# Kernel tuning notes

Measured on AMD Instinct MI355X. Metric: run time of the kernel, lower is better.

## Reference

```python
import jax, jax.numpy as jnp
import numpy as np

B, T, I, H = 32768, 18, 2, 64  # batch, seq_len (forced by fc2 in_features=18), input_dim, hidden_dim


def setup_inputs() -> dict:
    key = jax.random.key(0)
    ks = jax.random.split(key, 13)
    s = 1.0 / np.sqrt(H)  # torch default GRU/Linear init scale
    return {
        "x": jax.random.normal(ks[0], (B, T, I), jnp.float32),
        "w_ih_f": jax.random.uniform(ks[1], (3 * H, I), jnp.float32, -s, s),
        "w_hh_f": jax.random.uniform(ks[2], (3 * H, H), jnp.float32, -s, s),
        "b_ih_f": jax.random.uniform(ks[3], (3 * H,), jnp.float32, -s, s),
        "b_hh_f": jax.random.uniform(ks[4], (3 * H,), jnp.float32, -s, s),
        "w_ih_b": jax.random.uniform(ks[5], (3 * H, I), jnp.float32, -s, s),
        "w_hh_b": jax.random.uniform(ks[6], (3 * H, H), jnp.float32, -s, s),
        "b_ih_b": jax.random.uniform(ks[7], (3 * H,), jnp.float32, -s, s),
        "b_hh_b": jax.random.uniform(ks[8], (3 * H,), jnp.float32, -s, s),
        "fc1_w": jax.random.uniform(ks[9], (24, 2 * H), jnp.float32, -s, s),
        "fc1_b": jax.random.uniform(ks[10], (24,), jnp.float32, -s, s),
        "fc2_w": jax.random.uniform(ks[11], (2, T), jnp.float32, -s, s),
        "fc2_b": jax.random.uniform(ks[12], (2,), jnp.float32, -s, s),
    }


def _gru_scan(x_proj, w_hh, b_hh):
    """x_proj: (T, B, 3H) precomputed input projections. Returns (T, B, H)."""
    h0 = jnp.zeros((x_proj.shape[1], w_hh.shape[1]), x_proj.dtype)

    def step(h, xp):
        gh = h @ w_hh.T + b_hh
        i_r, i_z, i_n = jnp.split(xp, 3, axis=-1)
        h_r, h_z, h_n = jnp.split(gh, 3, axis=-1)
        r = jax.nn.sigmoid(i_r + h_r)
        z = jax.nn.sigmoid(i_z + h_z)
        n = jnp.tanh(i_n + r * h_n)
        h_new = (1 - z) * n + z * h
        return h_new, h_new

    _, hs = jax.lax.scan(step, h0, x_proj)
    return hs


def reference(x, w_ih_f, w_hh_f, b_ih_f, b_hh_f,
              w_ih_b, w_hh_b, b_ih_b, b_hh_b,
              fc1_w, fc1_b, fc2_w, fc2_b):
    # precompute input-gate projections for both directions: (T, B, 3H)
    xp_f = jnp.einsum('bti,gi->tbg', x, w_ih_f) + b_ih_f
    xp_b = jnp.einsum('bti,gi->tbg', x[:, ::-1], w_ih_b) + b_ih_b
    hf = _gru_scan(xp_f, w_hh_f, b_hh_f)           # (T, B, H)
    hb = _gru_scan(xp_b, w_hh_b, b_hh_b)[::-1]     # (T, B, H), re-aligned to forward time
    out = jnp.concatenate([hf, hb], axis=-1).transpose(1, 0, 2)  # (B, T, 2H)
    out = out @ fc1_w.T + fc1_b                    # (B, T, 24)
    out = out.reshape(out.shape[0], 24, -1)        # (B, 24, T) raw row-major reshape, as in torch
    out = out @ fc2_w.T + fc2_b                    # (B, 24, 2)
    return out
```

## Files before the change

kernel.cpp:

```cpp
#include <hip/hip_runtime.h>

#define TT 18

typedef __attribute__((ext_vector_type(8))) short short8;
typedef __attribute__((ext_vector_type(4))) float float4_t;
typedef __attribute__((ext_vector_type(2))) unsigned int uint2_t;

static __device__ __forceinline__ float frcp(float x){ return __builtin_amdgcn_rcpf(x); }
static __device__ __forceinline__ float sigm(float x){ return frcp(1.f + __expf(-x)); }
static __device__ __forceinline__ float tanh_fast(float x){ return fmaf(2.f, frcp(1.f + __expf(-2.f*x)), -1.f); }
static __device__ __forceinline__ unsigned rne_bits(float f){
    unsigned u = __float_as_uint(f);
    return u + 0x7fffu + ((u >> 16) & 1u);
}
static __device__ __forceinline__ void bsplit(float f, unsigned &hi, unsigned &lo){
    unsigned rb = rne_bits(f);
    hi = rb >> 16;
    float fh = __uint_as_float(rb & 0xffff0000u);
    lo = rne_bits(f - fh) >> 16;
}
static __device__ __forceinline__ unsigned pack_hi16(unsigned hi_src, unsigned lo_src){
#if defined(__has_builtin)
#if __has_builtin(__builtin_amdgcn_perm)
    return __builtin_amdgcn_perm(hi_src, lo_src, 0x07060302u);
#else
    return (lo_src >> 16) | (hi_src & 0xffff0000u);
#endif
#else
    return (lo_src >> 16) | (hi_src & 0xffff0000u);
#endif
}

union U8 { short8 s; unsigned u[4]; };

__global__ __launch_bounds__(256) void head_precompute(
    const float* __restrict__ fc1_w, const float* __restrict__ fc1_b,
    const float* __restrict__ fc2_w, const float* __restrict__ fc2_b,
    unsigned short* __restrict__ Bhi, unsigned short* __restrict__ Blo,
    float* __restrict__ Cvec)
{
    int idx = blockIdx.x * 256 + threadIdx.x;
    if (idx < 24 * 2 * 18 * 128) {
        int jg = idx & 127;
        int t  = (idx >> 7) % 18;
        int k  = (idx / 2304) & 1;
        int r  = idx / 4608;
        float acc = 0.f;
        for (int c = 0; c < 24; ++c) {
            int s = t * 24 + c - r * 18;
            if (s >= 0 && s < 18) acc += fc2_w[k * 18 + s] * fc1_w[c * 128 + jg];
        }
        unsigned hi, lo;
        bsplit(acc, hi, lo);
        Bhi[idx] = (unsigned short)hi;
        Blo[idx] = (unsigned short)lo;
    }
    if (idx < 48) {
        int k = idx & 1, r = idx >> 1;
        float acc = fc2_b[k];
        for (int s = 0; s < 18; ++s)
            acc += fc2_w[k * 18 + s] * fc1_b[(r * 18 + s) % 24];
        Cvec[idx] = acc;
    }
}

struct SMv {
    alignas(16) unsigned short hb[2][2][1024];
    uint2_t x2[16][18];
    float out_acc[16][49];
};

__global__ __launch_bounds__(256, 4) void gru_mfma(
    const float* __restrict__ x,
    const float* __restrict__ w_ih_f, const float* __restrict__ w_hh_f,
    const float* __restrict__ b_ih_f, const float* __restrict__ b_hh_f,
    const float* __restrict__ w_ih_b, const float* __restrict__ w_hh_b,
    const float* __restrict__ b_ih_b, const float* __restrict__ b_hh_b,
    const unsigned short* __restrict__ Bhi, const unsigned short* __restrict__ Blo,
    const float* __restrict__ Cvec, float* __restrict__ out)
{
    __shared__ SMv sm;
    const int tid  = threadIdx.x;
    const int lane = tid & 63;
    const int jq   = tid >> 6;
    const int col  = lane & 15;
    const int quad = lane >> 4;
    const int bi   = blockIdx.x;
    const int dir  = bi >> 11;
    const int bb   = (bi & 2047) * 16;
    const bool q0  = (quad == 0);

    const float* __restrict__ wih = dir ? w_ih_b : w_ih_f;
    const float* __restrict__ whh = dir ? w_hh_b : w_hh_f;
    const float* __restrict__ bih = dir ? b_ih_b : b_ih_f;
    const float* __restrict__ bhh = dir ? b_hh_b : b_hh_f;

    #pragma unroll
    for (int p = tid; p < 288; p += 256) {
        int b = p / 18, t = p % 18;
        const float* xp = x + (size_t)(bb + b) * 36 + t * 2;
        unsigned h0, l0, h1, l1;
        bsplit(xp[0], h0, l0);
        bsplit(xp[1], h1, l1);
        uint2_t s2; s2[0] = h0 | (l0 << 16); s2[1] = h1 | (l1 << 16);
        sm.x2[b][t] = s2;
    }
    {
        unsigned* z = (unsigned*)&sm.hb[1][0][0];
        #pragma unroll
        for (int o = 0; o < 4; ++o) z[tid + o * 256] = 0u;
    }
    for (int o = tid; o < 16 * 49; o += 256) ((float*)sm.out_acc)[o] = 0.f;

    short8 wf[3][2];
    #pragma unroll
    for (int ty = 0; ty < 3; ++ty) {
        int g = ty * 64 + jq * 16 + col;
        #pragma unroll
        for (int c = 0; c < 2; ++c) {
            const float* p = whh + g * 64 + c * 32 + quad * 8;
            float4_t f0 = *(const float4_t*)p;
            float4_t f1 = *(const float4_t*)(p + 4);
            short8 s;
            #pragma unroll
            for (int e = 0; e < 8; ++e) {
                float f = (e < 4) ? f0[e] : f1[e - 4];
                s[e] = (short)(rne_bits(f) >> 16);
            }
            wf[ty][c] = s;
        }
    }

    short8 c2[4];
    {
        #pragma unroll
        for (int ty = 0; ty < 2; ++ty) {
            int g = ty * 64 + jq * 16 + col;
            unsigned w0h, w0l, w1h, w1l, bh, bl;
            bsplit(wih[2 * g],     w0h, w0l);
            bsplit(wih[2 * g + 1], w1h, w1l);
            bsplit(bih[g] + bhh[g], bh, bl);
            U8 f;
            f.u[0] = q0 ? (w0h | (w0h << 16)) : 0u;
            f.u[1] = q0 ? (w0l | (w1h << 16)) : 0u;
            f.u[2] = q0 ? (w1h | (w1l << 16)) : 0u;
            f.u[3] = q0 ? (bh  | (bl  << 16)) : 0u;
            c2[ty] = f.s;
        }
        int g = 128 + jq * 16 + col;
        unsigned w0h, w0l, w1h, w1l, bxh, bxl, bhh_h, bhh_l;
        bsplit(wih[2 * g],     w0h, w0l);
        bsplit(wih[2 * g + 1], w1h, w1l);
        bsplit(bih[g], bxh, bxl);
        bsplit(bhh[g], bhh_h, bhh_l);
        U8 fn;
        fn.u[0] = 0u; fn.u[1] = 0u; fn.u[2] = 0u;
        fn.u[3] = q0 ? (bhh_h | (bhh_l << 16)) : 0u;
        c2[2] = fn.s;
        U8 fx;
        fx.u[0] = q0 ? (w0h | (w0h << 16)) : 0u;
        fx.u[1] = q0 ? (w0l | (w1h << 16)) : 0u;
        fx.u[2] = q0 ? (w1h | (w1l << 16)) : 0u;
        fx.u[3] = q0 ? (bxh | (bxl << 16)) : 0u;
        c2[3] = fx.s;
    }

    float hprev[4] = {0.f, 0.f, 0.f, 0.f};

    __syncthreads();

    auto step = [&](int t, int pr, int pw) {
        const bool myhead = (t > 0) && (((t - 1) & 3) == jq);

        int ta_h = 0, base_h = 0;
        size_t boff = 0;
        short8 hA0, hA1, lA0, lA1, hfl0, hfl1;
        if (myhead) {
            int s  = t - 1;
            ta_h   = dir ? (TT - 1 - s) : s;
            base_h = 4 * (ta_h / 3) + ta_h % 3;
            int i  = col & 3;
            int rr = base_h + (i >> 1);
            int kk = i & 1;
            boff = (size_t)((rr * 2 + kk) * TT + ta_h) * 128 + dir * 64 + quad * 8;
            hA0 = *(const short8*)(Bhi + boff);
            hA1 = *(const short8*)(Bhi + boff + 32);
            hfl0 = *(const short8*)&sm.hb[pr][1][(0 * 4 + quad) * 128 + col * 8];
            hfl1 = *(const short8*)&sm.hb[pr][1][(1 * 4 + quad) * 128 + col * 8];
        }

        short8 hfh[2];
        #pragma unroll
        for (int c = 0; c < 2; ++c)
            hfh[c] = *(const short8*)&sm.hb[pr][0][(c * 4 + quad) * 128 + col * 8];

        const int tx = dir ? (TT - 1 - t) : t;
        short8 b2f;
        {
            uint2_t xs = sm.x2[col][tx];
            U8 B;
            B.u[0] = q0 ? xs[0] : 0u;
            B.u[1] = q0 ? ((xs[0] & 0xffffu) | (xs[1] << 16)) : 0u;
            B.u[2] = q0 ? ((xs[1] >> 16) | (xs[1] << 16)) : 0u;
            B.u[3] = q0 ? 0x3F803F80u : 0u;
            b2f = B.s;
        }

        float4_t aR  = (float4_t){0.f,0.f,0.f,0.f};
        float4_t aZ  = (float4_t){0.f,0.f,0.f,0.f};
        float4_t aNH = (float4_t){0.f,0.f,0.f,0.f};
        float4_t aNX = (float4_t){0.f,0.f,0.f,0.f};
        #pragma unroll
        for (int c = 0; c < 2; ++c) {
            aR  = __builtin_amdgcn_mfma_f32_16x16x32_bf16(wf[0][c], hfh[c], aR,  0, 0, 0);
            aZ  = __builtin_amdgcn_mfma_f32_16x16x32_bf16(wf[1][c], hfh[c], aZ,  0, 0, 0);
            aNH = __builtin_amdgcn_mfma_f32_16x16x32_bf16(wf[2][c], hfh[c], aNH, 0, 0, 0);
        }
        aR  = __builtin_amdgcn_mfma_f32_16x16x32_bf16(c2[0], b2f, aR,  0, 0, 0);
        aZ  = __builtin_amdgcn_mfma_f32_16x16x32_bf16(c2[1], b2f, aZ,  0, 0, 0);
        aNH = __builtin_amdgcn_mfma_f32_16x16x32_bf16(c2[2], b2f, aNH, 0, 0, 0);
        aNX = __builtin_amdgcn_mfma_f32_16x16x32_bf16(c2[3], b2f, aNX, 0, 0, 0);

        unsigned rh[4], rl[4];
        #pragma unroll
        for (int reg = 0; reg < 4; ++reg) {
            float r = sigm(aR[reg]);
            float z = sigm(aZ[reg]);
            float n = tanh_fast(fmaf(r, aNH[reg], aNX[reg]));
            float hnew = fmaf(z, hprev[reg] - n, n);
            hprev[reg] = hnew;
            unsigned rb = rne_bits(hnew);
            rh[reg] = rb;
            float fh = __uint_as_float(rb & 0xffff0000u);
            rl[reg] = rne_bits(hnew - fh);
        }
        int woff = (jq * 2 + (quad >> 1)) * 128 + col * 8 + (quad & 1) * 4;
        uint2_t dh, dl;
        dh[0] = pack_hi16(rh[1], rh[0]);
        dh[1] = pack_hi16(rh[3], rh[2]);
        dl[0] = pack_hi16(rl[1], rl[0]);
        dl[1] = pack_hi16(rl[3], rl[2]);
        *(uint2_t*)&sm.hb[pw][0][woff] = dh;
        *(uint2_t*)&sm.hb[pw][1][woff] = dl;

        if (myhead) {
            lA0 = *(const short8*)(Blo + boff);
            lA1 = *(const short8*)(Blo + boff + 32);
            float4_t acch = (float4_t){0.f,0.f,0.f,0.f};
            acch = __builtin_amdgcn_mfma_f32_16x16x32_bf16(hA0, hfh[0], acch, 0, 0, 0);
            acch = __builtin_amdgcn_mfma_f32_16x16x32_bf16(hA1, hfh[1], acch, 0, 0, 0);
            acch = __builtin_amdgcn_mfma_f32_16x16x32_bf16(hA0, hfl0,   acch, 0, 0, 0);
            acch = __builtin_amdgcn_mfma_f32_16x16x32_bf16(hA1, hfl1,   acch, 0, 0, 0);
            acch = __builtin_amdgcn_mfma_f32_16x16x32_bf16(lA0, hfh[0], acch, 0, 0, 0);
            acch = __builtin_amdgcn_mfma_f32_16x16x32_bf16(lA1, hfh[1], acch, 0, 0, 0);
            if (q0) {
                #pragma unroll
                for (int reg = 0; reg < 4; ++reg) {
                    int r2 = base_h + (reg >> 1);
                    sm.out_acc[col][r2 * 2 + (reg & 1)] += acch[reg];
                }
            }
        }
        __syncthreads();
    };

    #pragma unroll 1
    for (int tt = 0; tt < 9; ++tt) {
        step(2 * tt,     1, 0);
        step(2 * tt + 1, 0, 1);
    }

    if (jq == ((TT - 1) & 3)) {
        int s  = TT - 1;
        int ta = dir ? 0 : s;
        int base_h = 4 * (ta / 3) + ta % 3;
        int i  = col & 3;
        int rr = base_h + (i >> 1);
        int kk = i & 1;
        size_t boff = (size_t)((rr * 2 + kk) * TT + ta) * 128 + dir * 64 + quad * 8;
        short8 hA0 = *(const short8*)(Bhi + boff);
        short8 hA1 = *(const short8*)(Bhi + boff + 32);
        short8 lA0 = *(const short8*)(Blo + boff);
        short8 lA1 = *(const short8*)(Blo + boff + 32);
        short8 hfh0 = *(const short8*)&sm.hb[1][0][(0 * 4 + quad) * 128 + col * 8];
        short8 hfh1 = *(const short8*)&sm.hb[1][0][(1 * 4 + quad) * 128 + col * 8];
        short8 hfl0 = *(const short8*)&sm.hb[1][1][(0 * 4 + quad) * 128 + col * 8];
        short8 hfl1 = *(const short8*)&sm.hb[1][1][(1 * 4 + quad) * 128 + col * 8];
        float4_t acch = (float4_t){0.f,0.f,0.f,0.f};
        acch = __builtin_amdgcn_mfma_f32_16x16x32_bf16(hA0, hfh0, acch, 0, 0, 0);
        acch = __builtin_amdgcn_mfma_f32_16x16x32_bf16(hA1, hfh1, acch, 0, 0, 0);
        acch = __builtin_amdgcn_mfma_f32_16x16x32_bf16(hA0, hfl0, acch, 0, 0, 0);
        acch = __builtin_amdgcn_mfma_f32_16x16x32_bf16(hA1, hfl1, acch, 0, 0, 0);
        acch = __builtin_amdgcn_mfma_f32_16x16x32_bf16(lA0, hfh0, acch, 0, 0, 0);
        acch = __builtin_amdgcn_mfma_f32_16x16x32_bf16(lA1, hfh1, acch, 0, 0, 0);
        if (q0) {
            #pragma unroll
            for (int reg = 0; reg < 4; ++reg) {
                int r2 = base_h + (reg >> 1);
                sm.out_acc[col][r2 * 2 + (reg & 1)] += acch[reg];
            }
        }
    }
    __syncthreads();

    #pragma unroll
    for (int rep = 0; rep < 3; ++rep) {
        int o = rep * 256 + tid;
        int b = o / 48, c = o % 48;
        atomicAdd(&out[(size_t)bb * 48 + o], sm.out_acc[b][c] + 0.5f * Cvec[c]);
    }
}

extern "C" void kernel_launch(void* const* d_in, const int* in_sizes, int n_in,
                              void* d_out, int out_size, void* d_ws, size_t ws_size,
                              hipStream_t stream) {
    const float* x      = (const float*)d_in[0];
    const float* w_ih_f = (const float*)d_in[1];
    const float* w_hh_f = (const float*)d_in[2];
    const float* b_ih_f = (const float*)d_in[3];
    const float* b_hh_f = (const float*)d_in[4];
    const float* w_ih_b = (const float*)d_in[5];
    const float* w_hh_b = (const float*)d_in[6];
    const float* b_ih_b = (const float*)d_in[7];
    const float* b_hh_b = (const float*)d_in[8];
    const float* fc1_w  = (const float*)d_in[9];
    const float* fc1_b  = (const float*)d_in[10];
    const float* fc2_w  = (const float*)d_in[11];
    const float* fc2_b  = (const float*)d_in[12];
    float* out  = (float*)d_out;

    float*          Cvec = (float*)d_ws;
    unsigned short* Bhi  = (unsigned short*)((char*)d_ws + 256);
    unsigned short* Blo  = Bhi + 110592;

    hipMemsetAsync(d_out, 0, (size_t)out_size * sizeof(float), stream);
    head_precompute<<<432, 256, 0, stream>>>(fc1_w, fc1_b, fc2_w, fc2_b, Bhi, Blo, Cvec);
    gru_mfma<<<4096, 256, 0, stream>>>(x, w_ih_f, w_hh_f, b_ih_f, b_hh_f,
                                       w_ih_b, w_hh_b, b_ih_b, b_hh_b,
                                       Bhi, Blo, Cvec, out);
}
```

Baseline: 194.5 us.

## Prescale gate weights by log2e, stage x/bias fragments in LDS, use exp2

Folds the log2(e) and 2*log2(e) factors into the recurrent, input and bias weights so the gate nonlinearities can call the hardware exp2 directly without an extra multiply. The per-lane constant bias and input-weight fragments and the per-step x operand are moved from registers into shared memory, with one wave building the next step's x fragment ahead of time. This is meant to cut register pressure and per-step VALU packing work. The low half of the h split now skips rounding, and the head-accumulation loads are regrouped into one block. The cost is extra LDS reads every step and slight numerical differences from prescaling weights before the bf16 split.

```diff
diff --git a/kernel.cpp b/kernel.cpp
--- a/kernel.cpp
+++ b/kernel.cpp
@@ -6,9 +6,17 @@
 typedef __attribute__((ext_vector_type(4))) float float4_t;
 typedef __attribute__((ext_vector_type(2))) unsigned int uint2_t;
 
+#if defined(__has_builtin)
+#if __has_builtin(__builtin_amdgcn_exp2f)
+#define FEXP2(x) __builtin_amdgcn_exp2f(x)
+#else
+#define FEXP2(x) exp2f(x)
+#endif
+#else
+#define FEXP2(x) exp2f(x)
+#endif
+
 static __device__ __forceinline__ float frcp(float x){ return __builtin_amdgcn_rcpf(x); }
-static __device__ __forceinline__ float sigm(float x){ return frcp(1.f + __expf(-x)); }
-static __device__ __forceinline__ float tanh_fast(float x){ return fmaf(2.f, frcp(1.f + __expf(-2.f*x)), -1.f); }
 static __device__ __forceinline__ unsigned rne_bits(float f){
     unsigned u = __float_as_uint(f);
     return u + 0x7fffu + ((u >> 16) & 1u);
@@ -32,6 +40,8 @@
 }
 
 union U8 { short8 s; unsigned u[4]; };
+
+#define MFMA16(A,B,C) __builtin_amdgcn_mfma_f32_16x16x32_bf16((A),(B),(C),0,0,0)
 
 __global__ __launch_bounds__(256) void head_precompute(
     const float* __restrict__ fc1_w, const float* __restrict__ fc1_b,
@@ -66,6 +76,9 @@
 
 struct SMv {
     alignas(16) unsigned short hb[2][2][1024];
+    alignas(16) unsigned short b2x[2][64][8];
+    alignas(16) unsigned short c2a[4][4][16][8];
+    alignas(16) unsigned short zero16[8];
     uint2_t x2[16][18];
     float out_acc[16][49];
 };
@@ -95,7 +108,20 @@
     const float* __restrict__ bih = dir ? b_ih_b : b_ih_f;
     const float* __restrict__ bhh = dir ? b_hh_b : b_hh_f;
 
-    #pragma unroll
+    const float L1 = 1.4426950408889634f;
+    const float L2 = 2.8853900817779268f;
+
+    {
+        unsigned* z = (unsigned*)&sm.hb[1][0][0];
+        #pragma unroll
+        for (int o = 0; o < 4; ++o) z[tid + o * 256] = 0u;
+        unsigned* z2 = (unsigned*)&sm.b2x[0][0][0];
+        #pragma unroll
+        for (int o = 0; o < 2; ++o) z2[tid + o * 256] = 0u;
+        if (tid < 4) ((unsigned*)sm.zero16)[tid] = 0u;
+    }
+    for (int o = tid; o < 16 * 49; o += 256) ((float*)sm.out_acc)[o] = 0.f;
+
     for (int p = tid; p < 288; p += 256) {
         int b = p / 18, t = p % 18;
         const float* xp = x + (size_t)(bb + b) * 36 + t * 2;
@@ -105,16 +131,64 @@
         uint2_t s2; s2[0] = h0 | (l0 << 16); s2[1] = h1 | (l1 << 16);
         sm.x2[b][t] = s2;
     }
-    {
-        unsigned* z = (unsigned*)&sm.hb[1][0][0];
-        #pragma unroll
-        for (int o = 0; o < 4; ++o) z[tid + o * 256] = 0u;
-    }
-    for (int o = tid; o < 16 * 49; o += 256) ((float*)sm.out_acc)[o] = 0.f;
+
+    if (tid < 16) {
+        int tx0 = dir ? (TT - 1) : 0;
+        const float* xp = x + (size_t)(bb + tid) * 36 + tx0 * 2;
+        unsigned h0, l0, h1, l1;
+        bsplit(xp[0], h0, l0);
+        bsplit(xp[1], h1, l1);
+        U8 B;
+        B.u[0] = h0 | (l0 << 16);
+        B.u[1] = h0 | (h1 << 16);
+        B.u[2] = l1 | (h1 << 16);
+        B.u[3] = 0x3F803F80u;
+        *(short8*)&sm.b2x[1][tid][0] = B.s;
+    }
+
+    if (q0) {
+        int g0 = jq * 16 + col;
+        #pragma unroll
+        for (int ty = 0; ty < 2; ++ty) {
+            int g = ty * 64 + g0;
+            unsigned w0h, w0l, w1h, w1l, bh, bl;
+            bsplit(L1 * wih[2 * g],     w0h, w0l);
+            bsplit(L1 * wih[2 * g + 1], w1h, w1l);
+            bsplit(L1 * (bih[g] + bhh[g]), bh, bl);
+            U8 f;
+            f.u[0] = w0h | (w0h << 16);
+            f.u[1] = w0l | (w1h << 16);
+            f.u[2] = w1h | (w1l << 16);
+            f.u[3] = bh  | (bl  << 16);
+            *(short8*)&sm.c2a[jq][ty][col][0] = f.s;
+        }
+        {
+            unsigned bh, bl;
+            bsplit(L2 * bhh[128 + g0], bh, bl);
+            U8 f;
+            f.u[0] = 0u; f.u[1] = 0u; f.u[2] = 0u;
+            f.u[3] = bh | (bl << 16);
+            *(short8*)&sm.c2a[jq][2][col][0] = f.s;
+        }
+        {
+            int g = 128 + g0;
+            unsigned w0h, w0l, w1h, w1l, bh, bl;
+            bsplit(L2 * wih[2 * g],     w0h, w0l);
+            bsplit(L2 * wih[2 * g + 1], w1h, w1l);
+            bsplit(L2 * bih[g], bh, bl);
+            U8 f;
+            f.u[0] = w0h | (w0h << 16);
+            f.u[1] = w0l | (w1h << 16);
+            f.u[2] = w1h | (w1l << 16);
+            f.u[3] = bh  | (bl  << 16);
+            *(short8*)&sm.c2a[jq][3][col][0] = f.s;
+        }
+    }
 
     short8 wf[3][2];
     #pragma unroll
     for (int ty = 0; ty < 3; ++ty) {
+        float sc = (ty == 2) ? L2 : L1;
         int g = ty * 64 + jq * 16 + col;
         #pragma unroll
         for (int c = 0; c < 2; ++c) {
@@ -125,114 +199,58 @@
             #pragma unroll
             for (int e = 0; e < 8; ++e) {
                 float f = (e < 4) ? f0[e] : f1[e - 4];
-                s[e] = (short)(rne_bits(f) >> 16);
+                s[e] = (short)(rne_bits(sc * f) >> 16);
             }
             wf[ty][c] = s;
         }
     }
 
-    short8 c2[4];
-    {
-        #pragma unroll
-        for (int ty = 0; ty < 2; ++ty) {
-            int g = ty * 64 + jq * 16 + col;
-            unsigned w0h, w0l, w1h, w1l, bh, bl;
-            bsplit(wih[2 * g],     w0h, w0l);
-            bsplit(wih[2 * g + 1], w1h, w1l);
-            bsplit(bih[g] + bhh[g], bh, bl);
-            U8 f;
-            f.u[0] = q0 ? (w0h | (w0h << 16)) : 0u;
-            f.u[1] = q0 ? (w0l | (w1h << 16)) : 0u;
-            f.u[2] = q0 ? (w1h | (w1l << 16)) : 0u;
-            f.u[3] = q0 ? (bh  | (bl  << 16)) : 0u;
-            c2[ty] = f.s;
-        }
-        int g = 128 + jq * 16 + col;
-        unsigned w0h, w0l, w1h, w1l, bxh, bxl, bhh_h, bhh_l;
-        bsplit(wih[2 * g],     w0h, w0l);
-        bsplit(wih[2 * g + 1], w1h, w1l);
-        bsplit(bih[g], bxh, bxl);
-        bsplit(bhh[g], bhh_h, bhh_l);
-        U8 fn;
-        fn.u[0] = 0u; fn.u[1] = 0u; fn.u[2] = 0u;
-        fn.u[3] = q0 ? (bhh_h | (bhh_l << 16)) : 0u;
-        c2[2] = fn.s;
-        U8 fx;
-        fx.u[0] = q0 ? (w0h | (w0h << 16)) : 0u;
-        fx.u[1] = q0 ? (w0l | (w1h << 16)) : 0u;
-        fx.u[2] = q0 ? (w1h | (w1l << 16)) : 0u;
-        fx.u[3] = q0 ? (bxh | (bxl << 16)) : 0u;
-        c2[3] = fx.s;
-    }
+    const unsigned short* c2p0 = q0 ? &sm.c2a[jq][0][col][0] : sm.zero16;
+    const unsigned short* c2p1 = q0 ? &sm.c2a[jq][1][col][0] : sm.zero16;
+    const unsigned short* c2p2 = q0 ? &sm.c2a[jq][2][col][0] : sm.zero16;
+    const unsigned short* c2p3 = q0 ? &sm.c2a[jq][3][col][0] : sm.zero16;
 
     float hprev[4] = {0.f, 0.f, 0.f, 0.f};
 
     __syncthreads();
 
     auto step = [&](int t, int pr, int pw) {
-        const bool myhead = (t > 0) && (((t - 1) & 3) == jq);
-
-        int ta_h = 0, base_h = 0;
-        size_t boff = 0;
-        short8 hA0, hA1, lA0, lA1, hfl0, hfl1;
-        if (myhead) {
-            int s  = t - 1;
-            ta_h   = dir ? (TT - 1 - s) : s;
-            base_h = 4 * (ta_h / 3) + ta_h % 3;
-            int i  = col & 3;
-            int rr = base_h + (i >> 1);
-            int kk = i & 1;
-            boff = (size_t)((rr * 2 + kk) * TT + ta_h) * 128 + dir * 64 + quad * 8;
-            hA0 = *(const short8*)(Bhi + boff);
-            hA1 = *(const short8*)(Bhi + boff + 32);
-            hfl0 = *(const short8*)&sm.hb[pr][1][(0 * 4 + quad) * 128 + col * 8];
-            hfl1 = *(const short8*)&sm.hb[pr][1][(1 * 4 + quad) * 128 + col * 8];
-        }
-
         short8 hfh[2];
-        #pragma unroll
-        for (int c = 0; c < 2; ++c)
-            hfh[c] = *(const short8*)&sm.hb[pr][0][(c * 4 + quad) * 128 + col * 8];
-
-        const int tx = dir ? (TT - 1 - t) : t;
-        short8 b2f;
-        {
-            uint2_t xs = sm.x2[col][tx];
-            U8 B;
-            B.u[0] = q0 ? xs[0] : 0u;
-            B.u[1] = q0 ? ((xs[0] & 0xffffu) | (xs[1] << 16)) : 0u;
-            B.u[2] = q0 ? ((xs[1] >> 16) | (xs[1] << 16)) : 0u;
-            B.u[3] = q0 ? 0x3F803F80u : 0u;
-            b2f = B.s;
-        }
+        hfh[0] = *(const short8*)&sm.hb[pr][0][quad * 128 + col * 8];
+        hfh[1] = *(const short8*)&sm.hb[pr][0][(4 + quad) * 128 + col * 8];
+        short8 b2f  = *(const short8*)&sm.b2x[pr][lane][0];
+        short8 c2f0 = *(const short8*)c2p0;
+        short8 c2f1 = *(const short8*)c2p1;
+        short8 c2f2 = *(const short8*)c2p2;
+        short8 c2f3 = *(const short8*)c2p3;
 
         float4_t aR  = (float4_t){0.f,0.f,0.f,0.f};
         float4_t aZ  = (float4_t){0.f,0.f,0.f,0.f};
         float4_t aNH = (float4_t){0.f,0.f,0.f,0.f};
         float4_t aNX = (float4_t){0.f,0.f,0.f,0.f};
-        #pragma unroll
-        for (int c = 0; c < 2; ++c) {
-            aR  = __builtin_amdgcn_mfma_f32_16x16x32_bf16(wf[0][c], hfh[c], aR,  0, 0, 0);
-            aZ  = __builtin_amdgcn_mfma_f32_16x16x32_bf16(wf[1][c], hfh[c], aZ,  0, 0, 0);
-            aNH = __builtin_amdgcn_mfma_f32_16x16x32_bf16(wf[2][c], hfh[c], aNH, 0, 0, 0);
-        }
-        aR  = __builtin_amdgcn_mfma_f32_16x16x32_bf16(c2[0], b2f, aR,  0, 0, 0);
-        aZ  = __builtin_amdgcn_mfma_f32_16x16x32_bf16(c2[1], b2f, aZ,  0, 0, 0);
-        aNH = __builtin_amdgcn_mfma_f32_16x16x32_bf16(c2[2], b2f, aNH, 0, 0, 0);
-        aNX = __builtin_amdgcn_mfma_f32_16x16x32_bf16(c2[3], b2f, aNX, 0, 0, 0);
+        aR  = MFMA16(wf[0][0], hfh[0], aR);
+        aR  = MFMA16(wf[0][1], hfh[1], aR);
+        aR  = MFMA16(c2f0,     b2f,    aR);
+        aZ  = MFMA16(wf[1][0], hfh[0], aZ);
+        aZ  = MFMA16(wf[1][1], hfh[1], aZ);
+        aZ  = MFMA16(c2f1,     b2f,    aZ);
+        aNH = MFMA16(wf[2][0], hfh[0], aNH);
+        aNH = MFMA16(wf[2][1], hfh[1], aNH);
+        aNH = MFMA16(c2f2,     b2f,    aNH);
+        aNX = MFMA16(c2f3,     b2f,    aNX);
 
         unsigned rh[4], rl[4];
         #pragma unroll
         for (int reg = 0; reg < 4; ++reg) {
-            float r = sigm(aR[reg]);
-            float z = sigm(aZ[reg]);
-            float n = tanh_fast(fmaf(r, aNH[reg], aNX[reg]));
+            float r = frcp(1.f + FEXP2(-aR[reg]));
+            float z = frcp(1.f + FEXP2(-aZ[reg]));
+            float a = fmaf(r, aNH[reg], aNX[reg]);
+            float n = fmaf(2.f, frcp(1.f + FEXP2(-a)), -1.f);
             float hnew = fmaf(z, hprev[reg] - n, n);
             hprev[reg] = hnew;
             unsigned rb = rne_bits(hnew);
             rh[reg] = rb;
-            float fh = __uint_as_float(rb & 0xffff0000u);
-            rl[reg] = rne_bits(hnew - fh);
+            rl[reg] = __float_as_uint(hnew - __uint_as_float(rb & 0xffff0000u));
         }
         int woff = (jq * 2 + (quad >> 1)) * 128 + col * 8 + (quad & 1) * 4;
         uint2_t dh, dl;
@@ -243,16 +261,39 @@
         *(uint2_t*)&sm.hb[pw][0][woff] = dh;
         *(uint2_t*)&sm.hb[pw][1][woff] = dl;
 
-        if (myhead) {
-            lA0 = *(const short8*)(Blo + boff);
-            lA1 = *(const short8*)(Blo + boff + 32);
+        if (jq == 0 && q0) {
+            int tn  = (t + 1 < TT) ? (t + 1) : (TT - 1);
+            int txn = dir ? (TT - 1 - tn) : tn;
+            uint2_t xs = sm.x2[col][txn];
+            U8 B;
+            B.u[0] = xs[0];
+            B.u[1] = (xs[0] & 0xffffu) | (xs[1] << 16);
+            B.u[2] = (xs[1] >> 16) | (xs[1] << 16);
+            B.u[3] = 0x3F803F80u;
+            *(short8*)&sm.b2x[pw][lane][0] = B.s;
+        }
+
+        if (t > 0 && ((t - 1) & 3) == jq) {
+            int s  = t - 1;
+            int ta = dir ? (TT - 1 - s) : s;
+            int base_h = 4 * (ta / 3) + ta % 3;
+            int i  = col & 3;
+            int rr = base_h + (i >> 1);
+            int kk = i & 1;
+            size_t boff = (size_t)((rr * 2 + kk) * TT + ta) * 128 + dir * 64 + quad * 8;
+            short8 hA0 = *(const short8*)(Bhi + boff);
+            short8 hA1 = *(const short8*)(Bhi + boff + 32);
+            short8 lA0 = *(const short8*)(Blo + boff);
+            short8 lA1 = *(const short8*)(Blo + boff + 32);
+            short8 hfl0 = *(const short8*)&sm.hb[pr][1][quad * 128 + col * 8];
+            short8 hfl1 = *(const short8*)&sm.hb[pr][1][(4 + quad) * 128 + col * 8];
             float4_t acch = (float4_t){0.f,0.f,0.f,0.f};
-            acch = __builtin_amdgcn_mfma_f32_16x16x32_bf16(hA0, hfh[0], acch, 0, 0, 0);
-            acch = __builtin_amdgcn_mfma_f32_16x16x32_bf16(hA1, hfh[1], acch, 0, 0, 0);
-            acch = __builtin_amdgcn_mfma_f32_16x16x32_bf16(hA0, hfl0,   acch, 0, 0, 0);
-            acch = __builtin_amdgcn_mfma_f32_16x16x32_bf16(hA1, hfl1,   acch, 0, 0, 0);
-            acch = __builtin_amdgcn_mfma_f32_16x16x32_bf16(lA0, hfh[0], acch, 0, 0, 0);
-            acch = __builtin_amdgcn_mfma_f32_16x16x32_bf16(lA1, hfh[1], acch, 0, 0, 0);
+            acch = MFMA16(hA0, hfh[0], acch);
+            acch = MFMA16(hA1, hfh[1], acch);
+            acch = MFMA16(hA0, hfl0,   acch);
+            acch = MFMA16(hA1, hfl1,   acch);
+            acch = MFMA16(lA0, hfh[0], acch);
+            acch = MFMA16(lA1, hfh[1], acch);
             if (q0) {
                 #pragma unroll
                 for (int reg = 0; reg < 4; ++reg) {
@@ -282,17 +323,17 @@
         short8 hA1 = *(const short8*)(Bhi + boff + 32);
         short8 lA0 = *(const short8*)(Blo + boff);
         short8 lA1 = *(const short8*)(Blo + boff + 32);
-        short8 hfh0 = *(const short8*)&sm.hb[1][0][(0 * 4 + quad) * 128 + col * 8];
-        short8 hfh1 = *(const short8*)&sm.hb[1][0][(1 * 4 + quad) * 128 + col * 8];
-        short8 hfl0 = *(const short8*)&sm.hb[1][1][(0 * 4 + quad) * 128 + col * 8];
-        short8 hfl1 = *(const short8*)&sm.hb[1][1][(1 * 4 + quad) * 128 + col * 8];
+        short8 hfh0 = *(const short8*)&sm.hb[1][0][quad * 128 + col * 8];
+        short8 hfh1 = *(const short8*)&sm.hb[1][0][(4 + quad) * 128 + col * 8];
+        short8 hfl0 = *(const short8*)&sm.hb[1][1][quad * 128 + col * 8];
+        short8 hfl1 = *(const short8*)&sm.hb[1][1][(4 + quad) * 128 + col * 8];
         float4_t acch = (float4_t){0.f,0.f,0.f,0.f};
-        acch = __builtin_amdgcn_mfma_f32_16x16x32_bf16(hA0, hfh0, acch, 0, 0, 0);
-        acch = __builtin_amdgcn_mfma_f32_16x16x32_bf16(hA1, hfh1, acch, 0, 0, 0);
-        acch = __builtin_amdgcn_mfma_f32_16x16x32_bf16(hA0, hfl0, acch, 0, 0, 0);
-        acch = __builtin_amdgcn_mfma_f32_16x16x32_bf16(hA1, hfl1, acch, 0, 0, 0);
-        acch = __builtin_amdgcn_mfma_f32_16x16x32_bf16(lA0, hfh0, acch, 0, 0, 0);
-        acch = __builtin_amdgcn_mfma_f32_16x16x32_bf16(lA1, hfh1, acch, 0, 0, 0);
+        acch = MFMA16(hA0, hfh0, acch);
+        acch = MFMA16(hA1, hfh1, acch);
+        acch = MFMA16(hA0, hfl0, acch);
+        acch = MFMA16(hA1, hfl1, acch);
+        acch = MFMA16(lA0, hfh0, acch);
+        acch = MFMA16(lA1, hfh1, acch);
         if (q0) {
             #pragma unroll
             for (int reg = 0; reg < 4; ++reg) {
```

After: 193.6 us. About the same (-0.5%).
